# Performance work log

Measured on AMD Instinct MI355X. Metric: run time of the kernel, lower is better.

## Reference

```python
import jax, jax.numpy as jnp
import numpy as np

R = 0.25
M = 0


def setup_inputs() -> dict:
    key = jax.random.key(0)
    k1, k2, k3, k4 = jax.random.split(key, 4)
    B, T_cmp, C = 2, 4096, 4096
    H, KVH, D, W = 32, 8, 128, 512
    return {
        "x_m": jax.random.normal(k1, (B, 2 * T_cmp, C), dtype=jnp.float32),
        "xm_cmp": jax.random.normal(k2, (B, T_cmp, C), dtype=jnp.float32),
        "q_w": jax.random.normal(k3, (B, H, W, D), dtype=jnp.float32),
        "km_cmp": jax.random.normal(k4, (B, KVH, T_cmp, D), dtype=jnp.float32),
    }


def reference(x_m, xm_cmp, q_w, km_cmp):
    B, T_cmp, C = xm_cmp.shape
    groups = q_w.shape[1] // km_cmp.shape[1]  # GQA repeat factor
    scaling = q_w.shape[-1] ** -0.5

    # importance_score: repeat kv heads, scaled-dot attention, softmax over keys,
    # sum over query positions, mean over heads -> [B, T_cmp]
    km = jnp.repeat(km_cmp, groups, axis=1)  # [B, H, T_cmp, D]
    scores = jnp.einsum('bhqd,bhkd->bhqk', q_w, km) * scaling
    weights = jax.nn.softmax(scores, axis=-1)
    importance = weights.sum(axis=2).mean(axis=1)  # [B, T_cmp]

    # select_indices: static top-k count
    k = min(int(R * T_cmp + M * (1 - R) / 2), T_cmp)
    _, idx = jax.lax.top_k(importance, k)  # [B, k]

    # interleave_selected: selected compressed tokens are replaced by their
    # two original tokens x_m[2t], x_m[2t+1]; others keep xm_cmp[t].
    b_idx = jnp.arange(B)[:, None]
    expand_mask = jnp.zeros((B, T_cmp), dtype=bool).at[b_idx, idx].set(True)
    sizes = jnp.where(expand_mask, 2, 1)
    start = jnp.cumsum(sizes, axis=1) - sizes  # output start position per token
    T_out = T_cmp + k

    first = jnp.where(expand_mask[..., None], x_m[:, ::2], xm_cmp)  # [B,T_cmp,C]
    second = x_m[:, 1::2]  # [B, T_cmp, C]
    pos2 = jnp.where(expand_mask, start + 1, T_out)  # non-expanded -> dummy slot

    y = jnp.zeros((B, T_out + 1, C), dtype=xm_cmp.dtype)
    y = y.at[b_idx, start].set(first)
    y = y.at[b_idx, pos2].set(second)
    return y[:, :T_out]
```

## Files before the change

kernel.cpp:

```cpp
#include <hip/hip_runtime.h>
#include <hip/hip_bf16.h>

#define B_    2
#define H_    32
#define KVH_  8
#define T_    4096
#define C_    4096
#define D_    128
#define W_    512
#define KTOP  1024
#define TOUT  (T_ + KTOP)
#define QB    64
#define NQB   (W_/QB)
#define TB    64
#define NTT   (T_/TB)
#define NPART (H_*NQB)
#define NBLK  (NQB*H_*B_)
#define SLOG2E 0.12751744f

typedef __attribute__((ext_vector_type(8))) _Float16 half8;
typedef __attribute__((ext_vector_type(4))) float f32x4;

__device__ __forceinline__ void gload16(const void* g, void* l) {
    __builtin_amdgcn_global_load_lds(
        (const __attribute__((address_space(1))) void*)g,
        (__attribute__((address_space(3))) void*)l, 16, 0, 0);
}

__global__ __launch_bounds__(256) void convert_k_kernel(
    const float* __restrict__ km, _Float16* __restrict__ Khw,
    _Float16* __restrict__ Klw)
{
    int g = blockIdx.x*256 + threadIdx.x;
    size_t e = (size_t)g*8;
    int d0 = (int)(e & 127);
    size_t row = e >> 7;
    int t = (int)(row & (T_-1));
    size_t bk = row >> 12;
    int r = t & 63, tt = t >> 6;
    size_t off = (bk<<19) + (size_t)tt*(TB*D_) + (size_t)r*D_ + (d0 ^ ((r&7)<<3));
    float4 v0 = *(const float4*)(km + e);
    float4 v1 = *(const float4*)(km + e + 4);
    float f[8] = {v0.x,v0.y,v0.z,v0.w,v1.x,v1.y,v1.z,v1.w};
    half8 hh, hl;
#pragma unroll
    for (int i = 0; i < 8; ++i) {
        _Float16 hi = (_Float16)f[i];
        hh[i] = hi;
        hl[i] = (_Float16)(f[i] - (float)hi);
    }
    *(half8*)&Khw[off] = hh;
    *(half8*)&Klw[off] = hl;
}

#define STAGE1(bufidx, tt)                                                  \
    {                                                                       \
        const _Float16* gh_ = gh0 + (size_t)(tt)*8192;                      \
        gload16(gh_,        &sKh[bufidx][wid][lane*8]);                     \
        gload16(gh_ + 512,  &sKh[bufidx][wid][512 + lane*8]);               \
        gload16(gh_ + 1024, &sKh[bufidx][wid][1024 + lane*8]);              \
        gload16(gh_ + 1536, &sKh[bufidx][wid][1536 + lane*8]);              \
    }

#define STAGE2(bufidx, tt)                                                  \
    {                                                                       \
        const _Float16* gh_ = gh0 + (size_t)(tt)*8192;                      \
        const _Float16* gl_ = gl0 + (size_t)(tt)*8192;                      \
        gload16(gh_,        &sKh[bufidx][wid][lane*8]);                     \
        gload16(gh_ + 512,  &sKh[bufidx][wid][512 + lane*8]);               \
        gload16(gh_ + 1024, &sKh[bufidx][wid][1024 + lane*8]);              \
        gload16(gh_ + 1536, &sKh[bufidx][wid][1536 + lane*8]);              \
        gload16(gl_,        &sKl[bufidx][wid][lane*8]);                     \
        gload16(gl_ + 512,  &sKl[bufidx][wid][512 + lane*8]);               \
        gload16(gl_ + 1024, &sKl[bufidx][wid][1024 + lane*8]);              \
        gload16(gl_ + 1536, &sKl[bufidx][wid][1536 + lane*8]);              \
    }

#define MFMA1(bufidx, acc)                                                  \
    {                                                                       \
        const _Float16* bKh = sKh[bufidx][wid];                             \
        __builtin_amdgcn_s_setprio(1);                                      \
        _Pragma("unroll")                                                   \
        for (int ks2 = 0; ks2 < 4; ++ks2) {                                 \
            const int off = li*D_ + ((ks2*32 + lg*8) ^ ((li & 7) << 3));    \
            half8 bh = *(const half8*)&bKh[off];                            \
            _Pragma("unroll")                                               \
            for (int mm = 0; mm < 4; ++mm)                                  \
                acc[mm] = __builtin_amdgcn_mfma_f32_16x16x32_f16(qh[mm][ks2], bh, acc[mm], 0,0,0); \
        }                                                                   \
        __builtin_amdgcn_s_setprio(0);                                      \
    }

#define MFMA3(bufidx, acc)                                                  \
    {                                                                       \
        const _Float16* bKh = sKh[bufidx][wid];                             \
        const _Float16* bKl = sKl[bufidx][wid];                             \
        __builtin_amdgcn_s_setprio(1);                                      \
        _Pragma("unroll")                                                   \
        for (int ks2 = 0; ks2 < 4; ++ks2) {                                 \
            const int off = li*D_ + ((ks2*32 + lg*8) ^ ((li & 7) << 3));    \
            half8 bh = *(const half8*)&bKh[off];                            \
            half8 bl = *(const half8*)&bKl[off];                            \
            _Pragma("unroll")                                               \
            for (int mm = 0; mm < 4; ++mm)                                  \
                acc[mm] = __builtin_amdgcn_mfma_f32_16x16x32_f16(qh[mm][ks2], bh, acc[mm], 0,0,0); \
            _Pragma("unroll")                                               \
            for (int mm = 0; mm < 4; ++mm)                                  \
                acc[mm] = __builtin_amdgcn_mfma_f32_16x16x32_f16(ql[mm][ks2], bh, acc[mm], 0,0,0); \
            _Pragma("unroll")                                               \
            for (int mm = 0; mm < 4; ++mm)                                  \
                acc[mm] = __builtin_amdgcn_mfma_f32_16x16x32_f16(qh[mm][ks2], bl, acc[mm], 0,0,0); \
        }                                                                   \
        __builtin_amdgcn_s_setprio(0);                                      \
    }

#define EXPACC(acc)                                                         \
    _Pragma("unroll")                                                       \
    for (int mm = 0; mm < 4; ++mm)                                          \
        _Pragma("unroll")                                                   \
        for (int j = 0; j < 4; ++j)                                         \
            lacc[mm][j] += __builtin_amdgcn_exp2f(acc[mm][j]);

#define EXPSTORE(acc, t)                                                    \
    {                                                                       \
        float x = 0.f;                                                      \
        _Pragma("unroll")                                                   \
        for (int mm = 0; mm < 4; ++mm)                                      \
            _Pragma("unroll")                                               \
            for (int j = 0; j < 4; ++j)                                     \
                x += __builtin_amdgcn_exp2f(acc[mm][j]) * rv[mm][j];        \
        x += __shfl_xor(x, 16); x += __shfl_xor(x, 32);                     \
        if (lg == 0)                                                        \
            partial[po + (size_t)(t)*TB + kg*16 + li] = x;                  \
    }

#define P1BODY(t, ACCD, ACCE)                                               \
    {                                                                       \
        STAGE1(((t)+1) & 1, (t)+1);                                         \
        asm volatile("s_waitcnt vmcnt(4)" ::: "memory");                    \
        MFMA1((t) & 1, ACCD);                                               \
        EXPACC(ACCE);                                                       \
    }

#define P2BODY(t, ACCD, ACCE)                                               \
    {                                                                       \
        STAGE2(((t)+1) & 1, (t)+1);                                         \
        asm volatile("s_waitcnt vmcnt(9)" ::: "memory");                    \
        MFMA3((t) & 1, ACCD);                                               \
        EXPSTORE(ACCE, (t)-1);                                              \
    }

#define ACCZERO(acc)                                                        \
    _Pragma("unroll")                                                       \
    for (int mm = 0; mm < 4; ++mm) acc[mm] = (f32x4){0.f,0.f,0.f,0.f};

__global__ __launch_bounds__(256, 2) void fused_imp_kernel(
    const float* __restrict__ q_w, const _Float16* __restrict__ Khw,
    const _Float16* __restrict__ Klw, float* __restrict__ partial)
{
    __shared__ __align__(16) _Float16 sKh[2][4][16*D_];
    __shared__ __align__(16) _Float16 sKl[2][4][16*D_];
    __shared__ float sL[4][QB];
    __shared__ float sR[QB];

    const int tid = threadIdx.x, wid = tid >> 6, lane = tid & 63;
    const int lg = lane >> 4, li = lane & 15;
    const int kg = wid;

    const int flat = blockIdx.x;
    const int xcd = flat & 7, m = flat >> 3;
    const int g = (m >> 5)*8 + xcd;
    const int r = m & 31;
    const int kvh = g & 7, b = g >> 3;
    const int hh = r >> 3, qb = r & 7;
    const int h = kvh*4 + hh;

    half8 qh[4][4], ql[4][4];
    {
        const float* qp0 = q_w + (((size_t)b*H_ + h)*W_ + qb*QB + li)*D_;
#pragma unroll
        for (int mm = 0; mm < 4; ++mm)
#pragma unroll
            for (int ks2 = 0; ks2 < 4; ++ks2) {
                const float* p = qp0 + mm*16*D_ + ks2*32 + lg*8;
                float4 v0 = *(const float4*)p;
                float4 v1 = *(const float4*)(p+4);
                float f[8] = {v0.x,v0.y,v0.z,v0.w,v1.x,v1.y,v1.z,v1.w};
#pragma unroll
                for (int e = 0; e < 8; ++e) {
                    float fs = f[e] * SLOG2E;
                    _Float16 hv = (_Float16)fs;
                    qh[mm][ks2][e] = hv;
                    ql[mm][ks2][e] = (_Float16)(fs - (float)hv);
                }
            }
    }

    const size_t kvoff = ((size_t)b*KVH_ + kvh) * ((size_t)T_*D_);
    const _Float16* gh0 = Khw + kvoff + (size_t)wid*2048 + (size_t)lane*8;
    const _Float16* gl0 = Klw + kvoff + (size_t)wid*2048 + (size_t)lane*8;

    float lacc[4][4] = {};
    f32x4 accA[4], accB[4];

    STAGE1(0, 0);
    STAGE1(1, 1);
    asm volatile("s_waitcnt vmcnt(4)" ::: "memory");
    ACCZERO(accA);
    MFMA1(0, accA);
    for (int t = 1; t < NTT-1; t += 2) {
        ACCZERO(accB);
        P1BODY(t,   accB, accA);
        ACCZERO(accA);
        P1BODY(t+1, accA, accB);
    }
    asm volatile("s_waitcnt vmcnt(0)" ::: "memory");
    ACCZERO(accB);
    MFMA1(1, accB);
    EXPACC(accA);
    EXPACC(accB);

#pragma unroll
    for (int mm = 0; mm < 4; ++mm)
#pragma unroll
        for (int j = 0; j < 4; ++j) {
            float v = lacc[mm][j];
            v += __shfl_xor(v, 1); v += __shfl_xor(v, 2);
            v += __shfl_xor(v, 4); v += __shfl_xor(v, 8);
            if (li == 0) sL[kg][mm*16 + lg*4 + j] = v;
        }
    __syncthreads();
    if (tid < QB) {
        float l = sL[0][tid] + sL[1][tid] + sL[2][tid] + sL[3][tid];
        sR[tid] = 1.0f / l;
    }
    __syncthreads();
    float rv[4][4];
#pragma unroll
    for (int mm = 0; mm < 4; ++mm)
#pragma unroll
        for (int j = 0; j < 4; ++j)
            rv[mm][j] = sR[mm*16 + lg*4 + j];

    const size_t po = (((size_t)(h*NQB + qb))*B_ + b)*T_;
    STAGE2(0, 0);
    STAGE2(1, 1);
    asm volatile("s_waitcnt vmcnt(8)" ::: "memory");
    ACCZERO(accA);
    MFMA3(0, accA);
    for (int t = 1; t < NTT-1; t += 2) {
        ACCZERO(accB);
        P2BODY(t,   accB, accA);
        ACCZERO(accA);
        P2BODY(t+1, accA, accB);
    }
    asm volatile("s_waitcnt vmcnt(1)" ::: "memory");
    ACCZERO(accB);
    MFMA3(1, accB);
    EXPSTORE(accA, NTT-2);
    EXPSTORE(accB, NTT-1);
}

__global__ __launch_bounds__(256) void imp_reduce_kernel(
    const float* __restrict__ partial, float* __restrict__ imp)
{
    int gid = blockIdx.x*256 + threadIdx.x;
    int b = gid >> 12, t = gid & (T_-1);
    float s = 0.f;
    for (int i = 0; i < NPART; ++i)
        s += partial[((size_t)(i*B_ + b))*T_ + t];
    imp[gid] = s * (1.0f/H_);
}

__global__ __launch_bounds__(1024) void topk_kernel(
    const float* __restrict__ imp, int* __restrict__ mask, int* __restrict__ start)
{
    __shared__ int hist[256];
    __shared__ int sa[1024], sb[1024];
    __shared__ int sbin, srem;
    const int tid = threadIdx.x, b = blockIdx.x;
    const int i0 = 4*tid;

    unsigned key[4];
#pragma unroll
    for (int j = 0; j < 4; ++j) {
        unsigned u = __float_as_uint(imp[b*T_ + i0 + j]);
        key[j] = (u & 0x80000000u) ? ~u : (u | 0x80000000u);
    }

    unsigned prefix = 0;
    int k_rem = KTOP;
#pragma unroll
    for (int sh = 24; sh >= 0; sh -= 8) {
        unsigned hi_mask = (sh == 24) ? 0u : (0xFFFFFFFFu << (sh + 8));
        if (tid < 256) hist[tid] = 0;
        __syncthreads();
#pragma unroll
        for (int j = 0; j < 4; ++j)
            if ((key[j] & hi_mask) == prefix)
                atomicAdd(&hist[(key[j] >> sh) & 255], 1);
        __syncthreads();
        if (tid == 0) {
            int acc = 0, bin = 255;
            for (; bin > 0; --bin) {
                int hv = hist[bin];
                if (acc + hv >= k_rem) break;
                acc += hv;
            }
            sbin = bin; srem = k_rem - acc;
        }
        __syncthreads();
        prefix |= ((unsigned)sbin) << sh;
        k_rem = srem;
        __syncthreads();
    }

    int m[4], eq[4];
#pragma unroll
    for (int j = 0; j < 4; ++j) {
        m[j]  = key[j] > prefix ? 1 : 0;
        eq[j] = (key[j] == prefix) ? 1 : 0;
    }
    int e4 = eq[0]+eq[1]+eq[2]+eq[3];
    sa[tid] = e4;
    __syncthreads();
    {
        int *src = sa, *dst = sb;
        for (int off = 1; off < 1024; off <<= 1) {
            int v = src[tid];
            if (tid >= off) v += src[tid - off];
            dst[tid] = v;
            __syncthreads();
            int* t2 = src; src = dst; dst = t2;
        }
        int r = src[tid] - e4;
#pragma unroll
        for (int j = 0; j < 4; ++j) {
            if (eq[j] && r < k_rem) m[j] = 1;
            r += eq[j];
        }
    }
    __syncthreads();
    int s4 = m[0]+m[1]+m[2]+m[3];
    sa[tid] = s4;
    __syncthreads();
    int *src = sa, *dst = sb;
    for (int off = 1; off < 1024; off <<= 1) {
        int v = src[tid];
        if (tid >= off) v += src[tid - off];
        dst[tid] = v;
        __syncthreads();
        int* t2 = src; src = dst; dst = t2;
    }
    int excl = src[tid] - s4;
    start[b*T_+i0+0] = i0+0 + excl;
    start[b*T_+i0+1] = i0+1 + excl + m[0];
    start[b*T_+i0+2] = i0+2 + excl + m[0]+m[1];
    start[b*T_+i0+3] = i0+3 + excl + m[0]+m[1]+m[2];
    mask[b*T_+i0+0] = m[0]; mask[b*T_+i0+1] = m[1];
    mask[b*T_+i0+2] = m[2]; mask[b*T_+i0+3] = m[3];
}

__global__ __launch_bounds__(256) void scatter_kernel(
    const float* __restrict__ x_m, const float* __restrict__ xm_cmp,
    const int* __restrict__ mask, const int* __restrict__ start,
    float* __restrict__ out)
{
    const int t = blockIdx.x, b = blockIdx.y, tid = threadIdx.x;
    const int mk = mask[b*T_+t];
    const int st = start[b*T_+t];
    const float* s1 = mk ? (x_m + ((size_t)b*2*T_ + 2*t)*C_)
                         : (xm_cmp + ((size_t)b*T_ + t)*C_);
    float4* d1 = (float4*)(out + ((size_t)b*TOUT + st)*C_);
    const float4* s1v = (const float4*)s1;
    for (int i = tid; i < C_/4; i += 256) d1[i] = s1v[i];
    if (mk) {
        const float4* s2v = (const float4*)(x_m + ((size_t)b*2*T_ + 2*t+1)*C_);
        float4* d2 = d1 + C_/4;
        for (int i = tid; i < C_/4; i += 256) d2[i] = s2v[i];
    }
}

extern "C" void kernel_launch(void* const* d_in, const int* in_sizes, int n_in,
                              void* d_out, int out_size, void* d_ws, size_t ws_size,
                              hipStream_t stream)
{
    (void)in_sizes; (void)n_in; (void)out_size; (void)ws_size;
    const float* x_m    = (const float*)d_in[0];
    const float* xm_cmp = (const float*)d_in[1];
    const float* q_w    = (const float*)d_in[2];
    const float* km     = (const float*)d_in[3];
    float* out = (float*)d_out;

    char* ws = (char*)d_ws;
    _Float16* Khw   = (_Float16*)ws;
    _Float16* Klw   = (_Float16*)(ws + 16777216);
    float* partial  = (float*)(ws + 33554432);
    float* imp      = (float*)(ws + 41943040);
    int*   mask     = (int*)  (ws + 41975808);
    int*   start    = (int*)  (ws + 42008576);

    convert_k_kernel<<<dim3(4096), dim3(256), 0, stream>>>(km, Khw, Klw);
    fused_imp_kernel<<<dim3(NBLK), dim3(256), 0, stream>>>(q_w, Khw, Klw, partial);
    imp_reduce_kernel<<<dim3((B_*T_)/256), dim3(256), 0, stream>>>(partial, imp);
    topk_kernel<<<dim3(B_), dim3(1024), 0, stream>>>(imp, mask, start);
    scatter_kernel<<<dim3(T_, B_), dim3(256), 0, stream>>>(x_m, xm_cmp, mask, start, out);
}
```

Baseline: 267.5 us.

## Load K fragments directly into registers instead of staging through LDS

The score kernel no longer stages K tiles into swizzled shared memory with async global-to-LDS loads. Each lane now reads its half8 K fragments straight from global memory into registers, double-buffered across tiles. The convert kernel drops the swizzled tiled layout and writes K in plain row-major order. This removes LDS traffic, the explicit waitcnt pipelining and the LDS footprint, at the cost of uncoalesced-ish 16-byte global loads per lane, more registers, and relying on the compiler to hide load latency.

```diff
diff --git a/kernel.cpp b/kernel.cpp
--- a/kernel.cpp
+++ b/kernel.cpp
@@ -21,24 +21,11 @@
 typedef __attribute__((ext_vector_type(8))) _Float16 half8;
 typedef __attribute__((ext_vector_type(4))) float f32x4;
 
-__device__ __forceinline__ void gload16(const void* g, void* l) {
-    __builtin_amdgcn_global_load_lds(
-        (const __attribute__((address_space(1))) void*)g,
-        (__attribute__((address_space(3))) void*)l, 16, 0, 0);
-}
-
 __global__ __launch_bounds__(256) void convert_k_kernel(
     const float* __restrict__ km, _Float16* __restrict__ Khw,
     _Float16* __restrict__ Klw)
 {
-    int g = blockIdx.x*256 + threadIdx.x;
-    size_t e = (size_t)g*8;
-    int d0 = (int)(e & 127);
-    size_t row = e >> 7;
-    int t = (int)(row & (T_-1));
-    size_t bk = row >> 12;
-    int r = t & 63, tt = t >> 6;
-    size_t off = (bk<<19) + (size_t)tt*(TB*D_) + (size_t)r*D_ + (d0 ^ ((r&7)<<3));
+    size_t e = ((size_t)blockIdx.x*256 + threadIdx.x) * 8;
     float4 v0 = *(const float4*)(km + e);
     float4 v1 = *(const float4*)(km + e + 4);
     float f[8] = {v0.x,v0.y,v0.z,v0.w,v1.x,v1.y,v1.z,v1.w};
@@ -49,67 +36,47 @@
         hh[i] = hi;
         hl[i] = (_Float16)(f[i] - (float)hi);
     }
-    *(half8*)&Khw[off] = hh;
-    *(half8*)&Klw[off] = hl;
-}
-
-#define STAGE1(bufidx, tt)                                                  \
+    *(half8*)&Khw[e] = hh;
+    *(half8*)&Klw[e] = hl;
+}
+
+#define LOADH(F, t)                                                         \
+    _Pragma("unroll")                                                       \
+    for (int ks2 = 0; ks2 < 4; ++ks2)                                       \
+        F[ks2] = *(const half8*)(kh + (size_t)(t)*8192 + ks2*32);
+
+#define LOADHL(FH, FL, t)                                                   \
+    _Pragma("unroll")                                                       \
+    for (int ks2 = 0; ks2 < 4; ++ks2) {                                     \
+        FH[ks2] = *(const half8*)(kh + (size_t)(t)*8192 + ks2*32);          \
+        FL[ks2] = *(const half8*)(kl + (size_t)(t)*8192 + ks2*32);          \
+    }
+
+#define MFMA1(F, acc)                                                       \
     {                                                                       \
-        const _Float16* gh_ = gh0 + (size_t)(tt)*8192;                      \
-        gload16(gh_,        &sKh[bufidx][wid][lane*8]);                     \
-        gload16(gh_ + 512,  &sKh[bufidx][wid][512 + lane*8]);               \
-        gload16(gh_ + 1024, &sKh[bufidx][wid][1024 + lane*8]);              \
-        gload16(gh_ + 1536, &sKh[bufidx][wid][1536 + lane*8]);              \
-    }
-
-#define STAGE2(bufidx, tt)                                                  \
+        __builtin_amdgcn_s_setprio(1);                                      \
+        _Pragma("unroll")                                                   \
+        for (int ks2 = 0; ks2 < 4; ++ks2)                                   \
+            _Pragma("unroll")                                               \
+            for (int mm = 0; mm < 4; ++mm)                                  \
+                acc[mm] = __builtin_amdgcn_mfma_f32_16x16x32_f16(qh[mm][ks2], F[ks2], acc[mm], 0,0,0); \
+        __builtin_amdgcn_s_setprio(0);                                      \
+    }
+
+#define MFMA3(FH, FL, acc)                                                  \
     {                                                                       \
-        const _Float16* gh_ = gh0 + (size_t)(tt)*8192;                      \
-        const _Float16* gl_ = gl0 + (size_t)(tt)*8192;                      \
-        gload16(gh_,        &sKh[bufidx][wid][lane*8]);                     \
-        gload16(gh_ + 512,  &sKh[bufidx][wid][512 + lane*8]);               \
-        gload16(gh_ + 1024, &sKh[bufidx][wid][1024 + lane*8]);              \
-        gload16(gh_ + 1536, &sKh[bufidx][wid][1536 + lane*8]);              \
-        gload16(gl_,        &sKl[bufidx][wid][lane*8]);                     \
-        gload16(gl_ + 512,  &sKl[bufidx][wid][512 + lane*8]);               \
-        gload16(gl_ + 1024, &sKl[bufidx][wid][1024 + lane*8]);              \
-        gload16(gl_ + 1536, &sKl[bufidx][wid][1536 + lane*8]);              \
-    }
-
-#define MFMA1(bufidx, acc)                                                  \
-    {                                                                       \
-        const _Float16* bKh = sKh[bufidx][wid];                             \
         __builtin_amdgcn_s_setprio(1);                                      \
         _Pragma("unroll")                                                   \
         for (int ks2 = 0; ks2 < 4; ++ks2) {                                 \
-            const int off = li*D_ + ((ks2*32 + lg*8) ^ ((li & 7) << 3));    \
-            half8 bh = *(const half8*)&bKh[off];                            \
             _Pragma("unroll")                                               \
             for (int mm = 0; mm < 4; ++mm)                                  \
-                acc[mm] = __builtin_amdgcn_mfma_f32_16x16x32_f16(qh[mm][ks2], bh, acc[mm], 0,0,0); \
-        }                                                                   \
-        __builtin_amdgcn_s_setprio(0);                                      \
-    }
-
-#define MFMA3(bufidx, acc)                                                  \
-    {                                                                       \
-        const _Float16* bKh = sKh[bufidx][wid];                             \
-        const _Float16* bKl = sKl[bufidx][wid];                             \
-        __builtin_amdgcn_s_setprio(1);                                      \
-        _Pragma("unroll")                                                   \
-        for (int ks2 = 0; ks2 < 4; ++ks2) {                                 \
-            const int off = li*D_ + ((ks2*32 + lg*8) ^ ((li & 7) << 3));    \
-            half8 bh = *(const half8*)&bKh[off];                            \
-            half8 bl = *(const half8*)&bKl[off];                            \
+                acc[mm] = __builtin_amdgcn_mfma_f32_16x16x32_f16(qh[mm][ks2], FH[ks2], acc[mm], 0,0,0); \
             _Pragma("unroll")                                               \
             for (int mm = 0; mm < 4; ++mm)                                  \
-                acc[mm] = __builtin_amdgcn_mfma_f32_16x16x32_f16(qh[mm][ks2], bh, acc[mm], 0,0,0); \
+                acc[mm] = __builtin_amdgcn_mfma_f32_16x16x32_f16(ql[mm][ks2], FH[ks2], acc[mm], 0,0,0); \
             _Pragma("unroll")                                               \
             for (int mm = 0; mm < 4; ++mm)                                  \
-                acc[mm] = __builtin_amdgcn_mfma_f32_16x16x32_f16(ql[mm][ks2], bh, acc[mm], 0,0,0); \
-            _Pragma("unroll")                                               \
-            for (int mm = 0; mm < 4; ++mm)                                  \
-                acc[mm] = __builtin_amdgcn_mfma_f32_16x16x32_f16(qh[mm][ks2], bl, acc[mm], 0,0,0); \
+                acc[mm] = __builtin_amdgcn_mfma_f32_16x16x32_f16(qh[mm][ks2], FL[ks2], acc[mm], 0,0,0); \
         }                                                                   \
         __builtin_amdgcn_s_setprio(0);                                      \
     }
@@ -134,22 +101,6 @@
             partial[po + (size_t)(t)*TB + kg*16 + li] = x;                  \
     }
 
-#define P1BODY(t, ACCD, ACCE)                                               \
-    {                                                                       \
-        STAGE1(((t)+1) & 1, (t)+1);                                         \
-        asm volatile("s_waitcnt vmcnt(4)" ::: "memory");                    \
-        MFMA1((t) & 1, ACCD);                                               \
-        EXPACC(ACCE);                                                       \
-    }
-
-#define P2BODY(t, ACCD, ACCE)                                               \
-    {                                                                       \
-        STAGE2(((t)+1) & 1, (t)+1);                                         \
-        asm volatile("s_waitcnt vmcnt(9)" ::: "memory");                    \
-        MFMA3((t) & 1, ACCD);                                               \
-        EXPSTORE(ACCE, (t)-1);                                              \
-    }
-
 #define ACCZERO(acc)                                                        \
     _Pragma("unroll")                                                       \
     for (int mm = 0; mm < 4; ++mm) acc[mm] = (f32x4){0.f,0.f,0.f,0.f};
@@ -158,8 +109,6 @@
     const float* __restrict__ q_w, const _Float16* __restrict__ Khw,
     const _Float16* __restrict__ Klw, float* __restrict__ partial)
 {
-    __shared__ __align__(16) _Float16 sKh[2][4][16*D_];
-    __shared__ __align__(16) _Float16 sKl[2][4][16*D_];
     __shared__ float sL[4][QB];
     __shared__ float sR[QB];
 
@@ -197,28 +146,24 @@
     }
 
     const size_t kvoff = ((size_t)b*KVH_ + kvh) * ((size_t)T_*D_);
-    const _Float16* gh0 = Khw + kvoff + (size_t)wid*2048 + (size_t)lane*8;
-    const _Float16* gl0 = Klw + kvoff + (size_t)wid*2048 + (size_t)lane*8;
+    const _Float16* kh = Khw + kvoff + (size_t)(kg*16 + li)*D_ + lg*8;
+    const _Float16* kl = Klw + kvoff + (size_t)(kg*16 + li)*D_ + lg*8;
 
     float lacc[4][4] = {};
-    f32x4 accA[4], accB[4];
-
-    STAGE1(0, 0);
-    STAGE1(1, 1);
-    asm volatile("s_waitcnt vmcnt(4)" ::: "memory");
-    ACCZERO(accA);
-    MFMA1(0, accA);
-    for (int t = 1; t < NTT-1; t += 2) {
-        ACCZERO(accB);
-        P1BODY(t,   accB, accA);
-        ACCZERO(accA);
-        P1BODY(t+1, accA, accB);
-    }
-    asm volatile("s_waitcnt vmcnt(0)" ::: "memory");
-    ACCZERO(accB);
-    MFMA1(1, accB);
-    EXPACC(accA);
-    EXPACC(accB);
+    half8 FA[4], FB[4];
+    f32x4 acc[4];
+
+    LOADH(FA, 0);
+    for (int t = 0; t < NTT; t += 2) {
+        LOADH(FB, t+1);
+        ACCZERO(acc);
+        MFMA1(FA, acc);
+        EXPACC(acc);
+        if (t + 2 < NTT) LOADH(FA, t+2);
+        ACCZERO(acc);
+        MFMA1(FB, acc);
+        EXPACC(acc);
+    }
 
 #pragma unroll
     for (int mm = 0; mm < 4; ++mm)
@@ -243,22 +188,18 @@
             rv[mm][j] = sR[mm*16 + lg*4 + j];
 
     const size_t po = (((size_t)(h*NQB + qb))*B_ + b)*T_;
-    STAGE2(0, 0);
-    STAGE2(1, 1);
-    asm volatile("s_waitcnt vmcnt(8)" ::: "memory");
-    ACCZERO(accA);
-    MFMA3(0, accA);
-    for (int t = 1; t < NTT-1; t += 2) {
-        ACCZERO(accB);
-        P2BODY(t,   accB, accA);
-        ACCZERO(accA);
-        P2BODY(t+1, accA, accB);
-    }
-    asm volatile("s_waitcnt vmcnt(1)" ::: "memory");
-    ACCZERO(accB);
-    MFMA3(1, accB);
-    EXPSTORE(accA, NTT-2);
-    EXPSTORE(accB, NTT-1);
+    half8 LA[4], LB[4];
+    LOADHL(FA, LA, 0);
+    for (int t = 0; t < NTT; t += 2) {
+        LOADHL(FB, LB, t+1);
+        ACCZERO(acc);
+        MFMA3(FA, LA, acc);
+        EXPSTORE(acc, t);
+        if (t + 2 < NTT) LOADHL(FA, LA, t+2);
+        ACCZERO(acc);
+        MFMA3(FB, LB, acc);
+        EXPSTORE(acc, t+1);
+    }
 }
 
 __global__ __launch_bounds__(256) void imp_reduce_kernel(
```

Result: slower. 318.7 us (+19.1%).
